# Optimization experiments

Hardware: AMD Instinct MI355X
Metric: run time of the kernel (lower is better)

## Reference

```python
import jax, jax.numpy as jnp
import numpy as np

N = 100000      # nodes
E = 1600000     # edges (avg degree 16)
IN = 128        # in_channels
H = 4           # heads
C = 32          # out_channels per head
NEG_SLOPE = 0.2 # PyG GATConv default


def setup_inputs() -> dict:
    key = jax.random.key(0)
    k = jax.random.split(key, 6)
    x = jax.random.normal(k[0], (N, IN), jnp.float32)
    edge_index = jax.random.randint(k[1], (2, E), 0, N, jnp.int32)
    # Learned params of GATConv: linear weight, per-head attention vectors, bias
    W = jax.random.normal(k[2], (IN, H * C), jnp.float32) / np.sqrt(IN)
    a_src = jax.random.normal(k[3], (H, C), jnp.float32) * 0.1
    a_dst = jax.random.normal(k[4], (H, C), jnp.float32) * 0.1
    bias = jnp.zeros((H * C,), jnp.float32)
    return {"x": x, "edge_index": edge_index, "W": W,
            "a_src": a_src, "a_dst": a_dst, "bias": bias}


def reference(x, edge_index, W, a_src, a_dst, bias):
    n = x.shape[0]
    # Linear transform, per-head view: [N, H, C]
    h = (x @ W).reshape(n, H, C)
    # Node-level attention halves: alpha_i = <h_i, a>  -> [N, H]
    alpha_src = jnp.einsum('nhc,hc->nh', h, a_src)
    alpha_dst = jnp.einsum('nhc,hc->nh', h, a_dst)
    # add_self_loops=True (PyG default)
    loops = jnp.arange(n, dtype=edge_index.dtype)
    src = jnp.concatenate([edge_index[0], loops])  # [E+N]
    dst = jnp.concatenate([edge_index[1], loops])
    # Edge attention logits with LeakyReLU: [E+N, H]
    e = jax.nn.leaky_relu(alpha_src[src] + alpha_dst[dst], NEG_SLOPE)
    # Numerically stable softmax over incoming edges of each destination node
    m = jax.ops.segment_max(e, dst, num_segments=n)          # [N, H]
    e = jnp.exp(e - m[dst])
    denom = jax.ops.segment_sum(e, dst, num_segments=n)      # [N, H]
    att = e / denom[dst]                                     # [E+N, H]
    # Weighted scatter-aggregate of source features: [N, H, C]
    out = jax.ops.segment_sum(att[:, :, None] * h[src], dst, num_segments=n)
    # concat=True: flatten heads, add bias
    return out.reshape(n, H * C) + bias
```

## Files before the change

kernel.cpp:

```cpp
#include <hip/hip_runtime.h>
#include <stdint.h>


#define NBLK 128
#define BKT 64

typedef __bf16 bf16x8 __attribute__((ext_vector_type(8)));
typedef float f32x4 __attribute__((ext_vector_type(4)));

__device__ __forceinline__ float lrelu(float x) { return x >= 0.f ? x : 0.2f * x; }
__device__ __forceinline__ float blo(unsigned u) { return __uint_as_float(u << 16); }
__device__ __forceinline__ float bhi(unsigned u) { return __uint_as_float(u & 0xffff0000u); }

__global__ __launch_bounds__(256) void k_wprep(const float* __restrict__ W, __bf16* __restrict__ Wt) {
  int idx = blockIdx.x * 256 + threadIdx.x;
  int nn = idx & 127, k = idx >> 7;
  Wt[nn * 128 + k] = (__bf16)W[k * 128 + nn];
}

__global__ __launch_bounds__(256) void k_mega(const float* __restrict__ x, const __bf16* __restrict__ Wt,
                                              const float* __restrict__ a_src, const float* __restrict__ a_dst,
                                              __bf16* __restrict__ h, float* __restrict__ asrc,
                                              float* __restrict__ adst,
                                              const int* __restrict__ ei, int* __restrict__ cnt2,
                                              int n, int e, int NB, int CE, int ngb) {
  __shared__ __align__(16) char Wl[32768];
  __shared__ __align__(16) __bf16 hbuf[4][16 * 64];
  int t = threadIdx.x;

  if ((int)blockIdx.x >= ngb) {
    int hblk = (int)blockIdx.x - ngb;
    int* hist = (int*)Wl;
    for (int j = t; j < NB; j += 256) hist[j] = 0;
    __syncthreads();
    int i0 = hblk * CE, i1 = min(e, i0 + CE);
    for (int i = i0 + t; i < i1; i += 256) atomicAdd(&hist[ei[e + i] >> 6], 1);
    __syncthreads();
    for (int j = t; j < NB; j += 256) cnt2[j * NBLK + hblk] = hist[j];
    return;
  }

  {
    const float4* s4 = (const float4*)Wt;
    for (int i = t; i < 2048; i += 256) {
      int f = i << 4;
      int nr = f >> 8, c = f & 255;
      *(float4*)(Wl + ((nr << 8) | (c ^ ((nr & 7) << 4)))) = s4[i];
    }
  }
  __syncthreads();
  int wv = t >> 6, lane = t & 63;
  int arow = lane & 15, ag = lane >> 4, c15 = lane & 15;
  float as_t[8], ad_t[8];
#pragma unroll
  for (int tile = 0; tile < 8; ++tile) {
    as_t[tile] = a_src[tile * 16 + c15];
    ad_t[tile] = a_dst[tile * 16 + c15];
  }
  int strip = blockIdx.x * 64 + wv * 16;
  int row = strip + arow;
  float4 fa[8];
  if (row < n) {
    const float4* xr = (const float4*)(x + (size_t)row * 128);
#pragma unroll
    for (int q = 0; q < 4; ++q) {
      fa[2 * q]     = xr[q * 8 + ag * 2];
      fa[2 * q + 1] = xr[q * 8 + ag * 2 + 1];
    }
  } else {
#pragma unroll
    for (int q = 0; q < 8; ++q) fa[q] = make_float4(0.f, 0.f, 0.f, 0.f);
  }
  bf16x8 af[4];
#pragma unroll
  for (int q = 0; q < 4; ++q) {
    af[q][0] = (__bf16)fa[2 * q].x;     af[q][1] = (__bf16)fa[2 * q].y;
    af[q][2] = (__bf16)fa[2 * q].z;     af[q][3] = (__bf16)fa[2 * q].w;
    af[q][4] = (__bf16)fa[2 * q + 1].x; af[q][5] = (__bf16)fa[2 * q + 1].y;
    af[q][6] = (__bf16)fa[2 * q + 1].z; af[q][7] = (__bf16)fa[2 * q + 1].w;
  }
  f32x4 acc[8];
#pragma unroll
  for (int tile = 0; tile < 8; ++tile) acc[tile] = (f32x4){0.f, 0.f, 0.f, 0.f};
#pragma unroll
  for (int q = 0; q < 4; ++q) {
    int gb = (q * 64) + (ag << 4);
#pragma unroll
    for (int tile = 0; tile < 8; ++tile) {
      int nn = tile * 16 + c15;
      bf16x8 bf = *(const bf16x8*)(Wl + ((nn << 8) | (gb ^ ((nn & 7) << 4))));
      acc[tile] = __builtin_amdgcn_mfma_f32_16x16x32_bf16(af[q], bf, acc[tile], 0, 0, 0);
    }
  }
#pragma unroll
  for (int hh = 0; hh < 4; ++hh) {
#pragma unroll
    for (int r = 0; r < 4; ++r) {
      float vps = acc[2 * hh][r] * as_t[2 * hh] + acc[2 * hh + 1][r] * as_t[2 * hh + 1];
      float vpd = acc[2 * hh][r] * ad_t[2 * hh] + acc[2 * hh + 1][r] * ad_t[2 * hh + 1];
#pragma unroll
      for (int m = 1; m < 16; m <<= 1) {
        vps += __shfl_xor(vps, m, 64);
        vpd += __shfl_xor(vpd, m, 64);
      }
      if (c15 == 0) {
        int ro = strip + ag * 4 + r;
        if (ro < n) { asrc[ro * 4 + hh] = vps; adst[ro * 4 + hh] = vpd; }
      }
    }
  }
  int rr = lane >> 2, qq = lane & 3;
  int ro = strip + rr;
#pragma unroll
  for (int half = 0; half < 2; ++half) {
#pragma unroll
    for (int tile = 0; tile < 4; ++tile) {
#pragma unroll
      for (int r = 0; r < 4; ++r)
        hbuf[wv][(ag * 4 + r) * 64 + tile * 16 + c15] = (__bf16)acc[half * 4 + tile][r];
    }
    if (ro < n) {
      const float4* src = (const float4*)&hbuf[wv][rr * 64 + qq * 16];
      float4* dst = (float4*)(h + (size_t)ro * 128 + half * 64 + qq * 16);
      dst[0] = src[0];
      dst[1] = src[1];
    }
  }
}


__global__ __launch_bounds__(256) void k_scanA(int* __restrict__ cnt2, int* __restrict__ bsums, int m) {
  __shared__ int wsum[4];
  int t = threadIdx.x, i = blockIdx.x * 256 + t;
  int wv = t >> 6, lane = t & 63;
  int v = (i < m) ? cnt2[i] : 0;
  int sc = v;
#pragma unroll
  for (int ofs = 1; ofs < 64; ofs <<= 1) {
    int u = __shfl_up(sc, ofs, 64);
    if (lane >= ofs) sc += u;
  }
  if (lane == 63) wsum[wv] = sc;
  __syncthreads();
  int base = 0;
  for (int w = 0; w < wv; ++w) base += wsum[w];
  if (i < m) cnt2[i] = base + sc - v;
  if (t == 255) bsums[blockIdx.x] = base + sc;
}

__global__ __launch_bounds__(256) void k_scanB(int* __restrict__ bsums, int nbs) {
  __shared__ int wsum[4];
  int t = threadIdx.x, wv = t >> 6, lane = t & 63;
  int carry = 0;
  for (int c = 0; c < nbs; c += 256) {
    int i = c + t;
    int v = (i < nbs) ? bsums[i] : 0;
    int sc = v;
#pragma unroll
    for (int ofs = 1; ofs < 64; ofs <<= 1) {
      int u = __shfl_up(sc, ofs, 64);
      if (lane >= ofs) sc += u;
    }
    if (lane == 63) wsum[wv] = sc;
    __syncthreads();
    int base = carry;
    for (int w = 0; w < wv; ++w) base += wsum[w];
    if (i < nbs) bsums[i] = base + sc - v;
    carry += wsum[0] + wsum[1] + wsum[2] + wsum[3];
    __syncthreads();
  }
}

__global__ __launch_bounds__(256) void k_fill2(const int* __restrict__ ei, const int* __restrict__ cnt2,
                                               const int* __restrict__ bsums,
                                               unsigned* __restrict__ ebuf, int e, int NB, int CE) {
  __shared__ int cur[2048];
  int t = threadIdx.x, blk = blockIdx.x;
  for (int j = t; j < NB; j += 256) {
    int idx = j * NBLK + blk;
    cur[j] = cnt2[idx] + bsums[idx >> 8];
  }
  __syncthreads();
  int i0 = blk * CE, i1 = min(e, i0 + CE);
  for (int i = i0 + t; i < i1; i += 256) {
    int s = ei[i], d = ei[e + i];
    int pos = atomicAdd(&cur[d >> 6], 1);
    ebuf[pos] = ((unsigned)(d & 63) << 26) | (unsigned)s;
  }
}

__global__ __launch_bounds__(256) void k_sort(const unsigned* __restrict__ ebuf, const int* __restrict__ cnt2,
                                              const int* __restrict__ bsums,
                                              int* __restrict__ off, int* __restrict__ adj, int n, int NB, int e) {
  __shared__ int lcnt[BKT], lcur[BKT];
  int b = blockIdx.x, t = threadIdx.x;
  int wv = t >> 6, lane = t & 63;
  int i0 = b * NBLK;
  int s0 = cnt2[i0] + bsums[i0 >> 8];
  int s1 = e;
  if (b + 1 < NB) { int i1 = (b + 1) * NBLK; s1 = cnt2[i1] + bsums[i1 >> 8]; }
  int cnt = s1 - s0;
  int d0 = b * BKT;
  if (t < BKT) lcnt[t] = 0;
  __syncthreads();
  for (int j = t; j < cnt; j += 256) atomicAdd(&lcnt[ebuf[s0 + j] >> 26], 1);
  __syncthreads();
  if (wv == 0) {
    int v = lcnt[lane];
    int sc = v;
#pragma unroll
    for (int o = 1; o < 64; o <<= 1) {
      int u = __shfl_up(sc, o, 64);
      if (lane >= o) sc += u;
    }
    lcur[lane] = sc - v;
    if (d0 + lane < n) off[d0 + lane] = s0 + sc - v;
  }
  if (b == 0 && t == 0) off[n] = e;
  __syncthreads();
  for (int j = t; j < cnt; j += 256) {
    unsigned u = ebuf[s0 + j];
    int pos = atomicAdd(&lcur[u >> 26], 1);
    adj[s0 + pos] = (int)(u & 0x03FFFFFFu);
  }
}

__global__ __launch_bounds__(256) void k_gather(const int* __restrict__ adj, const int* __restrict__ off,
                                                const float* __restrict__ asrc, const float* __restrict__ adst,
                                                const unsigned* __restrict__ h32,
                                                const float* __restrict__ bias, float* __restrict__ out, int n) {
  int gid = blockIdx.x * 256 + threadIdx.x;
  int node = gid >> 6, lane = gid & 63;
  if (node >= n) return;
  int head = lane >> 4;
  int o = off[node], oe = off[node + 1];
  float adh = adst[node * 4 + head];
  float ps = __expf(lrelu(asrc[node * 4 + head] + adh));
  unsigned su = h32[((unsigned)node << 6) + lane];
  float acc0 = ps * blo(su), acc1 = ps * bhi(su), dtot = ps;
  int j = o;
  for (; j + 8 <= oe; j += 8) {
    int sv[8];
    unsigned hu[8];
    float av[8];
#pragma unroll
    for (int k = 0; k < 8; ++k) sv[k] = adj[j + k];
#pragma unroll
    for (int k = 0; k < 8; ++k) {
      hu[k] = h32[((unsigned)sv[k] << 6) + lane];
      av[k] = asrc[sv[k] * 4 + head];
    }
#pragma unroll
    for (int k = 0; k < 8; ++k) {
      float p = __expf(lrelu(av[k] + adh));
      dtot += p;
      acc0 += p * blo(hu[k]);
      acc1 += p * bhi(hu[k]);
    }
  }
  for (; j + 2 <= oe; j += 2) {
    int sA = adj[j], sB = adj[j + 1];
    unsigned uA = h32[((unsigned)sA << 6) + lane];
    unsigned uB = h32[((unsigned)sB << 6) + lane];
    float pA = __expf(lrelu(asrc[sA * 4 + head] + adh));
    float pB = __expf(lrelu(asrc[sB * 4 + head] + adh));
    dtot += pA + pB;
    acc0 += pA * blo(uA) + pB * blo(uB);
    acc1 += pA * bhi(uA) + pB * bhi(uB);
  }
  if (j < oe) {
    int s = adj[j];
    unsigned u = h32[((unsigned)s << 6) + lane];
    float p = __expf(lrelu(asrc[s * 4 + head] + adh));
    dtot += p;
    acc0 += p * blo(u);
    acc1 += p * bhi(u);
  }
  float inv = 1.f / dtot;
  float2 bb = ((const float2*)bias)[lane];
  ((float2*)(out + (size_t)node * 128))[lane] = make_float2(acc0 * inv + bb.x, acc1 * inv + bb.y);
}

extern "C" void kernel_launch(void* const* d_in, const int* in_sizes, int n_in,
                              void* d_out, int out_size, void* d_ws, size_t ws_size,
                              hipStream_t stream) {
  const float* x     = (const float*)d_in[0];
  const int*   ei    = (const int*)d_in[1];
  const float* W     = (const float*)d_in[2];
  const float* a_src = (const float*)d_in[3];
  const float* a_dst = (const float*)d_in[4];
  const float* bias  = (const float*)d_in[5];
  float* out = (float*)d_out;

  int n = in_sizes[0] / 128;
  int e = in_sizes[1] / 2;
  int NB = (n + BKT - 1) / BKT;
  int ngb = (n + 63) / 64;
  int m = NB * NBLK;
  int gridA = (m + 255) / 256;
  int CE = (e + NBLK - 1) / NBLK;

  char* ws = (char*)d_ws;
  size_t ofs = 0;
  auto alloc = [&](size_t bytes) { void* p = ws + ofs; ofs = (ofs + bytes + 15) & ~(size_t)15; return p; };
  __bf16* h      = (__bf16*)alloc((size_t)n * 128 * sizeof(__bf16));
  unsigned* h32  = (unsigned*)h;
  float* asrc    = (float*)alloc((size_t)n * 4 * sizeof(float));
  float* adst    = (float*)alloc((size_t)n * 4 * sizeof(float));
  int* off       = (int*)alloc((size_t)(n + 1) * sizeof(int));
  int* cnt2      = (int*)alloc((size_t)m * sizeof(int));
  int* bsums     = (int*)alloc((size_t)gridA * sizeof(int));
  unsigned* ebuf = (unsigned*)alloc((size_t)e * sizeof(unsigned));
  int* adj       = (int*)alloc((size_t)e * sizeof(int));
  __bf16* Wt     = (__bf16*)alloc((size_t)128 * 128 * sizeof(__bf16));

  hipLaunchKernelGGL(k_wprep, dim3(64), dim3(256), 0, stream, W, Wt);
  hipLaunchKernelGGL(k_mega, dim3(ngb + NBLK), dim3(256), 0, stream,
                     x, Wt, a_src, a_dst, h, asrc, adst, ei, cnt2, n, e, NB, CE, ngb);
  hipLaunchKernelGGL(k_scanA, dim3(gridA), dim3(256), 0, stream, cnt2, bsums, m);
  hipLaunchKernelGGL(k_scanB, dim3(1), dim3(256), 0, stream, bsums, gridA);
  hipLaunchKernelGGL(k_fill2, dim3(NBLK), dim3(256), 0, stream, ei, cnt2, bsums, ebuf, e, NB, CE);
  hipLaunchKernelGGL(k_sort, dim3(NB), dim3(256), 0, stream, ebuf, cnt2, bsums, off, adj, n, NB, e);
  hipLaunchKernelGGL(k_gather, dim3((n * 64 + 255) / 256), dim3(256), 0, stream,
                     adj, off, asrc, adst, h32, bias, out, n);
}
```

Baseline: 163.7 us.

## Compute attention logits from bf16-rounded h and widen gather unroll to 12

The per-node attention scalars alpha_src and alpha_dst were computed from the fp32 MFMA accumulators with 16-lane shuffle reductions. They are now computed from the bf16 values already staged in LDS, so they match the stored h, and each dot product needs only one cross-half shuffle. The gather loop also unrolls by 12 instead of 8 and adds a 4-wide tail, which keeps more independent neighbor loads in flight. The risks are extra LDS reads and scalar a_src/a_dst loads in the epilogue, more register pressure in the gather, and small numeric differences from using bf16 h in the logits.

```diff
diff --git a/kernel.cpp b/kernel.cpp
--- a/kernel.cpp
+++ b/kernel.cpp
@@ -51,12 +51,6 @@
   __syncthreads();
   int wv = t >> 6, lane = t & 63;
   int arow = lane & 15, ag = lane >> 4, c15 = lane & 15;
-  float as_t[8], ad_t[8];
-#pragma unroll
-  for (int tile = 0; tile < 8; ++tile) {
-    as_t[tile] = a_src[tile * 16 + c15];
-    ad_t[tile] = a_dst[tile * 16 + c15];
-  }
   int strip = blockIdx.x * 64 + wv * 16;
   int row = strip + arow;
   float4 fa[8];
@@ -92,25 +86,11 @@
       acc[tile] = __builtin_amdgcn_mfma_f32_16x16x32_bf16(af[q], bf, acc[tile], 0, 0, 0);
     }
   }
-#pragma unroll
-  for (int hh = 0; hh < 4; ++hh) {
-#pragma unroll
-    for (int r = 0; r < 4; ++r) {
-      float vps = acc[2 * hh][r] * as_t[2 * hh] + acc[2 * hh + 1][r] * as_t[2 * hh + 1];
-      float vpd = acc[2 * hh][r] * ad_t[2 * hh] + acc[2 * hh + 1][r] * ad_t[2 * hh + 1];
-#pragma unroll
-      for (int m = 1; m < 16; m <<= 1) {
-        vps += __shfl_xor(vps, m, 64);
-        vpd += __shfl_xor(vpd, m, 64);
-      }
-      if (c15 == 0) {
-        int ro = strip + ag * 4 + r;
-        if (ro < n) { asrc[ro * 4 + hh] = vps; adst[ro * 4 + hh] = vpd; }
-      }
-    }
-  }
   int rr = lane >> 2, qq = lane & 3;
   int ro = strip + rr;
+  int row16 = lane & 15;
+  int hh2 = (lane >> 4) & 1;
+  int chunk = lane >> 5;
 #pragma unroll
   for (int half = 0; half < 2; ++half) {
 #pragma unroll
@@ -124,6 +104,24 @@
       float4* dst = (float4*)(h + (size_t)ro * 128 + half * 64 + qq * 16);
       dst[0] = src[0];
       dst[1] = src[1];
+    }
+    int headg = half * 2 + hh2;
+    const unsigned* hrow = (const unsigned*)&hbuf[wv][row16 * 64 + hh2 * 32 + chunk * 16];
+    const float* asv = a_src + headg * 32 + chunk * 16;
+    const float* adv = a_dst + headg * 32 + chunk * 16;
+    float ps = 0.f, pd = 0.f;
+#pragma unroll
+    for (int c = 0; c < 8; ++c) {
+      unsigned u = hrow[c];
+      float lo = blo(u), hi = bhi(u);
+      ps += lo * asv[2 * c] + hi * asv[2 * c + 1];
+      pd += lo * adv[2 * c] + hi * adv[2 * c + 1];
+    }
+    ps += __shfl_xor(ps, 32, 64);
+    pd += __shfl_xor(pd, 32, 64);
+    if (chunk == 0) {
+      int ro2 = strip + row16;
+      if (ro2 < n) { asrc[ro2 * 4 + headg] = ps; adst[ro2 * 4 + headg] = pd; }
     }
   }
 }
@@ -239,36 +237,45 @@
   unsigned su = h32[((unsigned)node << 6) + lane];
   float acc0 = ps * blo(su), acc1 = ps * bhi(su), dtot = ps;
   int j = o;
-  for (; j + 8 <= oe; j += 8) {
-    int sv[8];
-    unsigned hu[8];
-    float av[8];
-#pragma unroll
-    for (int k = 0; k < 8; ++k) sv[k] = adj[j + k];
-#pragma unroll
-    for (int k = 0; k < 8; ++k) {
+  for (; j + 12 <= oe; j += 12) {
+    int sv[12];
+    unsigned hu[12];
+    float av[12];
+#pragma unroll
+    for (int k = 0; k < 12; ++k) sv[k] = adj[j + k];
+#pragma unroll
+    for (int k = 0; k < 12; ++k) {
       hu[k] = h32[((unsigned)sv[k] << 6) + lane];
       av[k] = asrc[sv[k] * 4 + head];
     }
 #pragma unroll
-    for (int k = 0; k < 8; ++k) {
+    for (int k = 0; k < 12; ++k) {
       float p = __expf(lrelu(av[k] + adh));
       dtot += p;
       acc0 += p * blo(hu[k]);
       acc1 += p * bhi(hu[k]);
     }
   }
-  for (; j + 2 <= oe; j += 2) {
-    int sA = adj[j], sB = adj[j + 1];
-    unsigned uA = h32[((unsigned)sA << 6) + lane];
-    unsigned uB = h32[((unsigned)sB << 6) + lane];
-    float pA = __expf(lrelu(asrc[sA * 4 + head] + adh));
-    float pB = __expf(lrelu(asrc[sB * 4 + head] + adh));
-    dtot += pA + pB;
-    acc0 += pA * blo(uA) + pB * blo(uB);
-    acc1 += pA * bhi(uA) + pB * bhi(uB);
-  }
-  if (j < oe) {
+  for (; j + 4 <= oe; j += 4) {
+    int sv[4];
+    unsigned hu[4];
+    float av[4];
+#pragma unroll
+    for (int k = 0; k < 4; ++k) sv[k] = adj[j + k];
+#pragma unroll
+    for (int k = 0; k < 4; ++k) {
+      hu[k] = h32[((unsigned)sv[k] << 6) + lane];
+      av[k] = asrc[sv[k] * 4 + head];
+    }
+#pragma unroll
+    for (int k = 0; k < 4; ++k) {
+      float p = __expf(lrelu(av[k] + adh));
+      dtot += p;
+      acc0 += p * blo(hu[k]);
+      acc1 += p * bhi(hu[k]);
+    }
+  }
+  for (; j < oe; ++j) {
     int s = adj[j];
     unsigned u = h32[((unsigned)s << 6) + lane];
     float p = __expf(lrelu(asrc[s * 4 + head] + adh));
```

New measurement: 162.3 us. Within noise of the previous version (-0.8%).
